# Kernel tuning notes

Measured on AMD Instinct MI355X. Metric: run time of the kernel, lower is better.

## Reference

```python
import jax, jax.numpy as jnp
import numpy as np

N_NODES = 100000


def _gcn_conv(h, src, dst, norm, W, b, n):
    # linear transform then symmetric-normalized scatter-add aggregation
    hw = h @ W                                   # [N, out]
    msg = hw[src] * norm[:, None]                # [E+N, out] gathered messages
    out = jax.ops.segment_sum(msg, dst, num_segments=n)
    return out + b


def _self_loops_and_norm(edge_index, n):
    loop = jnp.arange(n, dtype=edge_index.dtype)
    src = jnp.concatenate([edge_index[0], loop])
    dst = jnp.concatenate([edge_index[1], loop])
    deg = jax.ops.segment_sum(jnp.ones_like(src, dtype=jnp.float32), dst, num_segments=n)
    dinv = jnp.where(deg > 0, jax.lax.rsqrt(jnp.maximum(deg, 1.0)), 0.0)
    norm = dinv[src] * dinv[dst]                 # D^-1/2 (A+I) D^-1/2 coefficients
    return src, dst, norm


def setup_inputs() -> dict:
    key = jax.random.key(0)
    k1, k2, k3, k4 = jax.random.split(key, 4)
    F_IN, H, C = 128, 64, 40
    x = jax.random.normal(k1, (N_NODES, F_IN), dtype=jnp.float32)
    edge_index = jax.random.randint(k2, (2, 3200000), 0, N_NODES, dtype=jnp.int64)
    s1 = 1.0 / np.sqrt(F_IN)
    s2 = 1.0 / np.sqrt(H)
    W1 = jax.random.uniform(k3, (F_IN, H), jnp.float32, -s1, s1)
    b1 = jnp.zeros((H,), jnp.float32)
    W2 = jax.random.uniform(k4, (H, C), jnp.float32, -s2, s2)
    b2 = jnp.zeros((C,), jnp.float32)
    return {"x": x, "edge_index": edge_index, "W1": W1, "b1": b1, "W2": W2, "b2": b2}


def reference(x, edge_index, W1, b1, W2, b2):
    n = x.shape[0]
    src, dst, norm = _self_loops_and_norm(edge_index, n)
    h = _gcn_conv(x, src, dst, norm, W1, b1, n)
    h = jax.nn.relu(h)
    # dropout(p=0.5) is identity in eval mode
    out = _gcn_conv(h, src, dst, norm, W2, b2, n)
    return jax.nn.log_softmax(out, axis=1)
```

## Files before the change

kernel.cpp:

```cpp
#include <hip/hip_runtime.h>
#include <math.h>

#define F_IN 128
#define HID  64
#define NCLS 40
#define PART_CHUNK 4096
#define CAP 4608
#define CAPX 768
#define MAXNB 1024
#define ASTRIDE 132

typedef _Float16 half8 __attribute__((ext_vector_type(8)));
typedef _Float16 half2t __attribute__((ext_vector_type(2)));
typedef float floatx4 __attribute__((ext_vector_type(4)));

__device__ inline half8 ld_half8_u8(const _Float16* p) {
    union { uint2 u[2]; half8 h; } r;
    r.u[0] = *(const uint2*)p;
    r.u[1] = *(const uint2*)(p + 4);
    return r.h;
}

__global__ __launch_bounds__(256) void fused_part_gemm1(const int* __restrict__ src,
                                                        const int* __restrict__ dst,
                                                        int* __restrict__ bCur,
                                                        int* __restrict__ pkBuf,
                                                        int E, int NB, int nPart,
                                                        const float* __restrict__ x,
                                                        const float* __restrict__ W1,
                                                        _Float16* __restrict__ h1, int n) {
    __shared__ __align__(16) char smem[2 * 64 * ASTRIDE * 2];
    int tid = threadIdx.x;
    if ((int)blockIdx.x < nPart) {
        int xcd = (int)blockIdx.x & 7;
        int* hcnt  = (int*)smem;
        int* hbase = (int*)smem + MAXNB;
        for (int i = tid; i < NB; i += 256) hcnt[i] = 0;
        __syncthreads();
        int e0 = blockIdx.x * PART_CHUNK;
        int s_[16], d_[16];
#pragma unroll
        for (int i = 0; i < 16; ++i) {
            int e = e0 + i * 256 + tid;
            if (e < E) {
                s_[i] = src[e]; d_[i] = dst[e];
                atomicAdd(&hcnt[d_[i] >> 7], 1);
            }
        }
        __syncthreads();
        for (int b = tid; b < NB; b += 256) {
            int c = hcnt[b];
            hbase[b] = c ? ((b * 8 + xcd) * CAPX + atomicAdd(&bCur[b * 8 + xcd], c)) : 0;
            hcnt[b] = 0;
        }
        __syncthreads();
#pragma unroll
        for (int i = 0; i < 16; ++i) {
            int e = e0 + i * 256 + tid;
            if (e < E) {
                int b = d_[i] >> 7;
                int loc = atomicAdd(&hcnt[b], 1);
                pkBuf[hbase[b] + loc] = (s_[i] << 7) | (d_[i] & 127);
            }
        }
    } else {
        _Float16* Ah = (_Float16*)smem;
        _Float16* Wt = Ah + 64 * ASTRIDE;
        int node0 = ((int)blockIdx.x - nPart) * 64;
#pragma unroll
        for (int i = 0; i < 8; ++i) {
            int f = (i * 256 + tid) * 4;
            int m = f >> 7, k = f & 127;
            float4 v = (node0 + m < n) ? ((const float4*)(x + (size_t)(node0 + m) * F_IN))[k >> 2]
                                       : make_float4(0.f, 0.f, 0.f, 0.f);
            _Float16* p = &Ah[m * ASTRIDE + k];
            p[0] = (_Float16)v.x; p[1] = (_Float16)v.y; p[2] = (_Float16)v.z; p[3] = (_Float16)v.w;
        }
#pragma unroll
        for (int i = 0; i < 32; ++i) {
            int f = i * 256 + tid;
            int k = f >> 6, nn = f & 63;
            Wt[nn * ASTRIDE + k] = (_Float16)W1[f];
        }
        __syncthreads();
        int wave = tid >> 6, lane = tid & 63;
        int m0 = wave * 16;
        int col = lane & 15, quad = lane >> 4;
        floatx4 acc[4] = {{0,0,0,0},{0,0,0,0},{0,0,0,0},{0,0,0,0}};
#pragma unroll
        for (int kk = 0; kk < 4; ++kk) {
            int kbase = kk * 32 + quad * 8;
            half8 a = ld_half8_u8(&Ah[(m0 + col) * ASTRIDE + kbase]);
#pragma unroll
            for (int t = 0; t < 4; ++t) {
                half8 b = ld_half8_u8(&Wt[(t * 16 + col) * ASTRIDE + kbase]);
                acc[t] = __builtin_amdgcn_mfma_f32_16x16x32_f16(a, b, acc[t], 0, 0, 0);
            }
        }
#pragma unroll
        for (int t = 0; t < 4; ++t)
#pragma unroll
            for (int r = 0; r < 4; ++r) {
                int node = node0 + m0 + quad * 4 + r;
                if (node < n) h1[(size_t)node * HID + t * 16 + col] = (_Float16)acc[t][r];
            }
    }
}

__global__ __launch_bounds__(256) void scan_buckets(const int* __restrict__ bCur,
                                                    int* __restrict__ bBase, int NB, int E) {
    __shared__ int part[256];
    int tid = threadIdx.x;
    int v[4]; int sum = 0;
#pragma unroll
    for (int k = 0; k < 4; ++k) {
        int i = tid * 4 + k;
        int s = 0;
        if (i < NB) {
#pragma unroll
            for (int x = 0; x < 8; ++x) s += bCur[i * 8 + x];
        }
        v[k] = s;
        sum += s;
    }
    part[tid] = sum; __syncthreads();
    for (int off = 1; off < 256; off <<= 1) {
        int t = (tid >= off) ? part[tid - off] : 0;
        __syncthreads();
        part[tid] += t;
        __syncthreads();
    }
    int base = part[tid] - sum;
#pragma unroll
    for (int k = 0; k < 4; ++k) {
        int i = tid * 4 + k;
        if (i < NB) bBase[i] = base;
        base += v[k];
    }
    if (tid == 255) bBase[NB] = E;
}

__global__ __launch_bounds__(256) void bucket_finalize(const int* __restrict__ bCur,
                                                       const int* __restrict__ bBase,
                                                       const int* __restrict__ pkBuf,
                                                       int* __restrict__ ptr,
                                                       float* __restrict__ dinv,
                                                       int* __restrict__ sIdx,
                                                       _Float16* __restrict__ h1,
                                                       int n, int E) {
    __shared__ int cnt128[128];
    __shared__ int sc[128];
    __shared__ int cur[128];
    __shared__ float sdinv[128];
    __shared__ int segoff[9];
    __shared__ int ebuf[CAP];
    __shared__ int stage[CAP];
    int b = blockIdx.x;
    int node0 = b << 7;
    int tid = threadIdx.x;
    if (tid < 128) cnt128[tid] = 0;
    if (tid == 0) {
        int o = 0;
#pragma unroll
        for (int x = 0; x < 8; ++x) { segoff[x] = o; o += bCur[b * 8 + x]; }
        segoff[8] = o;
    }
    __syncthreads();
    int cnt = segoff[8];
    int dbase = bBase[b];
    for (int x = 0; x < 8; ++x) {
        int off = segoff[x], len = segoff[x + 1] - off;
        const int* s = pkBuf + (size_t)(b * 8 + x) * CAPX;
        for (int j = tid; j < len; j += 256) {
            int p = s[j];
            ebuf[off + j] = p;
            atomicAdd(&cnt128[p & 127], 1);
        }
    }
    __syncthreads();
    int v = (tid < 128) ? cnt128[tid] : 0;
    if (tid < 128) sc[tid] = v;
    __syncthreads();
    for (int off = 1; off < 128; off <<= 1) {
        int t = (tid < 128 && tid >= off) ? sc[tid - off] : 0;
        __syncthreads();
        if (tid < 128) sc[tid] += t;
        __syncthreads();
    }
    if (tid < 128) {
        cur[tid] = sc[tid] - v;
        float dv = rsqrtf((float)v + 1.0f);
        sdinv[tid] = dv;
        int node = node0 + tid;
        if (node < n) {
            ptr[node] = dbase + sc[tid] - v;
            dinv[node] = dv;
        }
    }
    if (tid == 0 && b == gridDim.x - 1) ptr[n] = E;
    __syncthreads();
    for (int j = tid; j < cnt; j += 256) {
        int p = ebuf[j];
        int pos = atomicAdd(&cur[p & 127], 1);
        stage[pos] = p >> 7;
    }
    __syncthreads();
    for (int j = tid; j < cnt; j += 256)
        sIdx[dbase + j] = stage[j];
#pragma unroll
    for (int pass = 0; pass < 4; ++pass) {
        int idx = pass * 256 + tid;
        int nd = node0 + (idx >> 3);
        if (nd < n) {
            float dv = sdinv[idx >> 3];
            half8* p = (half8*)(h1 + (size_t)nd * HID) + (idx & 7);
            half8 hv = *p;
#pragma unroll
            for (int j = 0; j < 8; ++j) hv[j] = (_Float16)((float)hv[j] * dv);
            *p = hv;
        }
    }
}

template<bool RELU>
__global__ __launch_bounds__(256) void gather4(const int* __restrict__ ptr,
                                               const int* __restrict__ sIdx,
                                               const float* __restrict__ dinv,
                                               const _Float16* __restrict__ hin,
                                               const float* __restrict__ bias,
                                               _Float16* __restrict__ hout, int n) {
    int tid = threadIdx.x, wave = tid >> 6, lane = tid & 63;
    int ng   = lane >> 4;
    int slot = (lane >> 3) & 1;
    int fq   = lane & 7;
    int node = blockIdx.x * 16 + wave * 4 + ng;
    bool valid = node < n;
    int nodeC = valid ? node : 0;
    int beg = ptr[nodeC];
    int end = valid ? ptr[nodeC + 1] : beg;
    float di = dinv[nodeC];
    float a0[8] = {0,0,0,0,0,0,0,0}, a1[8] = {0,0,0,0,0,0,0,0};

    if (slot == 0 && valid) {
        half8 v = *(const half8*)(hin + nodeC * HID + fq * 8);
#pragma unroll
        for (int j = 0; j < 8; ++j) a0[j] = (float)v[j];
    }
    const _Float16 ONE = (_Float16)1.0f, ZEROH = (_Float16)0.0f;
    for (int j0 = beg; j0 < end; j0 += 8) {
        int ja = j0 + slot, jb = j0 + 2 + slot, jc = j0 + 4 + slot, jd = j0 + 6 + slot;
        bool va = ja < end, vb = jb < end, vc = jc < end, vd = jd < end;
        int sa = sIdx[va ? ja : beg];
        int sb = sIdx[vb ? jb : beg];
        int sc_ = sIdx[vc ? jc : beg];
        int sd = sIdx[vd ? jd : beg];
        half8 ra = *(const half8*)(hin + sa * HID + fq * 8);
        half8 rb = *(const half8*)(hin + sb * HID + fq * 8);
        half8 rc = *(const half8*)(hin + sc_ * HID + fq * 8);
        half8 rd = *(const half8*)(hin + sd * HID + fq * 8);
#if __has_builtin(__builtin_amdgcn_fdot2)
        half2t wab = { va ? ONE : ZEROH, vb ? ONE : ZEROH };
        half2t wcd = { vc ? ONE : ZEROH, vd ? ONE : ZEROH };
#pragma unroll
        for (int j = 0; j < 8; ++j) {
            half2t pab = { ra[j], rb[j] };
            half2t pcd = { rc[j], rd[j] };
            a0[j] = __builtin_amdgcn_fdot2(pab, wab, a0[j], false);
            a1[j] = __builtin_amdgcn_fdot2(pcd, wcd, a1[j], false);
        }
#else
        float wa = va ? 1.f : 0.f, wb = vb ? 1.f : 0.f, wc = vc ? 1.f : 0.f, wd = vd ? 1.f : 0.f;
#pragma unroll
        for (int j = 0; j < 8; ++j) {
            a0[j] = fmaf((float)ra[j], wa, a0[j]);
            a0[j] = fmaf((float)rb[j], wb, a0[j]);
            a1[j] = fmaf((float)rc[j], wc, a1[j]);
            a1[j] = fmaf((float)rd[j], wd, a1[j]);
        }
#endif
    }
#pragma unroll
    for (int j = 0; j < 8; ++j) {
        a0[j] += a1[j];
        a0[j] += __shfl_xor(a0[j], 8, 64);
    }
    if (slot == 0 && valid) {
        union { half8 h; uint4 u; } o;
#pragma unroll
        for (int j = 0; j < 8; ++j) {
            float v = di * a0[j];
            if (RELU) v = fmaxf(v + bias[fq * 8 + j], 0.f) * di;
            o.h[j] = (_Float16)v;
        }
        *(uint4*)(hout + nodeC * HID + fq * 8) = o.u;
    }
}

#define GSTRIDE 72
__global__ __launch_bounds__(256) void gemm2_mfma_logsm(const _Float16* __restrict__ g,
                                                        const float* __restrict__ W2,
                                                        const float* __restrict__ b2,
                                                        float* __restrict__ out, int n) {
    __shared__ _Float16 gt[64 * GSTRIDE];
    __shared__ _Float16 wt[48 * GSTRIDE];
    int tid = threadIdx.x;
    int node0 = blockIdx.x * 64;
#pragma unroll
    for (int i = 0; i < 2; ++i) {
        int f = (i * 256 + tid) * 8;
        int m = f >> 6, k = f & 63;
        union { uint4 u; half8 h; } v;
        if (node0 + m < n) v.u = *(const uint4*)(g + (size_t)(node0 + m) * HID + k);
        else v.u = make_uint4(0, 0, 0, 0);
        *(uint4*)&gt[m * GSTRIDE + k] = v.u;
    }
#pragma unroll
    for (int i = 0; i < 12; ++i) {
        int f = i * 256 + tid;
        int c = f >> 6, k = f & 63;
        wt[c * GSTRIDE + k] = (c < NCLS) ? (_Float16)W2[k * NCLS + c] : (_Float16)0.f;
    }
    __syncthreads();

    int wave = tid >> 6, lane = tid & 63;
    int m0 = wave * 16;
    int col = lane & 15, quad = lane >> 4;
    floatx4 acc[3] = {{0,0,0,0},{0,0,0,0},{0,0,0,0}};
#pragma unroll
    for (int kk = 0; kk < 2; ++kk) {
        int kbase = kk * 32 + quad * 8;
        half8 a = *(const half8*)&gt[(m0 + col) * GSTRIDE + kbase];
#pragma unroll
        for (int t = 0; t < 3; ++t) {
            half8 b = *(const half8*)&wt[(t * 16 + col) * GSTRIDE + kbase];
            acc[t] = __builtin_amdgcn_mfma_f32_16x16x32_f16(a, b, acc[t], 0, 0, 0);
        }
    }
    float bb[3];
#pragma unroll
    for (int t = 0; t < 3; ++t) {
        int c = t * 16 + col;
        bb[t] = (c < NCLS) ? b2[c] : 0.f;
    }
#pragma unroll
    for (int r = 0; r < 4; ++r) {
        int node = node0 + m0 + quad * 4 + r;
        float v0 = acc[0][r] + bb[0];
        float v1 = acc[1][r] + bb[1];
        float v2 = (col < 8) ? acc[2][r] + bb[2] : -INFINITY;
        float m = fmaxf(fmaxf(v0, v1), v2);
#pragma unroll
        for (int off = 1; off < 16; off <<= 1) m = fmaxf(m, __shfl_xor(m, off, 64));
        float s = expf(v0 - m) + expf(v1 - m) + ((col < 8) ? expf(v2 - m) : 0.f);
#pragma unroll
        for (int off = 1; off < 16; off <<= 1) s += __shfl_xor(s, off, 64);
        float ls = logf(s);
        if (node < n) {
            float* op = out + (size_t)node * NCLS;
            op[col]      = v0 - m - ls;
            op[16 + col] = v1 - m - ls;
            if (col < 8) op[32 + col] = v2 - m - ls;
        }
    }
}

extern "C" void kernel_launch(void* const* d_in, const int* in_sizes, int n_in,
                              void* d_out, int out_size, void* d_ws, size_t ws_size,
                              hipStream_t stream) {
    const float* x  = (const float*)d_in[0];
    const int*   ei = (const int*)d_in[1];
    const float* W1 = (const float*)d_in[2];
    const float* b1 = (const float*)d_in[3];
    const float* W2 = (const float*)d_in[4];
    const float* b2 = (const float*)d_in[5];
    float* out = (float*)d_out;

    int n = in_sizes[0] / F_IN;
    int E = in_sizes[1] / 2;
    const int* src = ei;
    const int* dst = ei + E;
    int NB = (n + 127) >> 7;
    int nPart = (E + PART_CHUNK - 1) / PART_CHUNK;
    int nGemm1 = (n + 63) / 64;

    char* ws = (char*)d_ws;
    const size_t MB = 1024 * 1024;
    int*      bCur  = (int*)  (ws);
    int*      bBase = (int*)  (ws + 64 * 1024);
    int*      ptr   = (int*)  (ws + 128 * 1024);
    float*    dinv  = (float*)(ws + 1 * MB);
    int*      sIdx  = (int*)     (ws + 2 * MB);
    _Float16* bufA  = (_Float16*)(ws + 15 * MB);
    int*      pkBuf = (int*)     (ws + 28 * MB);
    _Float16* bufB  = (_Float16*)(ws + 28 * MB);

    hipMemsetAsync(bCur, 0, (size_t)NB * 8 * sizeof(int), stream);
    fused_part_gemm1<<<nPart + nGemm1, 256, 0, stream>>>(src, dst, bCur, pkBuf, E, NB, nPart,
                                                         x, W1, bufA, n);
    scan_buckets<<<1, 256, 0, stream>>>(bCur, bBase, NB, E);
    bucket_finalize<<<NB, 256, 0, stream>>>(bCur, bBase, pkBuf, ptr, dinv, sIdx, bufA, n, E);

    gather4<true ><<<(n + 15) / 16, 256, 0, stream>>>(ptr, sIdx, dinv, bufA, b1, bufB, n);
    gather4<false><<<(n + 15) / 16, 256, 0, stream>>>(ptr, sIdx, dinv, bufB, b1, bufA, n);
    gemm2_mfma_logsm<<<(n + 63) / 64, 256, 0, stream>>>(bufA, W2, b2, out, n);
}
```

Measured before the change: 299.6 us.

## Split hidden features into four 16-wide planes for cache-local gathers

Changes the hidden-feature buffer layout from node-major [N,64] to four feature planes [4][N][16]. GEMM1, the dinv scaling, and GEMM2 are updated to match. Each gather block now handles one plane, so the random-access working set per pass (about 3.2 MB) is meant to fit in L2/LLC. The cost is reading the edge index list four times per layer, partly offset by nontemporal loads of the index. The gather loop is also simplified, with edges split across four slots, a tail step, and a shuffle reduction.

```diff
diff --git a/kernel.cpp b/kernel.cpp
--- a/kernel.cpp
+++ b/kernel.cpp
@@ -13,6 +13,8 @@
 typedef _Float16 half8 __attribute__((ext_vector_type(8)));
 typedef _Float16 half2t __attribute__((ext_vector_type(2)));
 typedef float floatx4 __attribute__((ext_vector_type(4)));
+typedef unsigned int uint4v __attribute__((ext_vector_type(4)));
+
 
 __device__ inline half8 ld_half8_u8(const _Float16* p) {
     union { uint2 u[2]; half8 h; } r;
@@ -102,7 +104,7 @@
 #pragma unroll
             for (int r = 0; r < 4; ++r) {
                 int node = node0 + m0 + quad * 4 + r;
-                if (node < n) h1[(size_t)node * HID + t * 16 + col] = (_Float16)acc[t][r];
+                if (node < n) h1[((size_t)t * n + node) * 16 + col] = (_Float16)acc[t][r];
             }
     }
 }
@@ -208,91 +210,95 @@
     for (int j = tid; j < cnt; j += 256)
         sIdx[dbase + j] = stage[j];
 #pragma unroll
-    for (int pass = 0; pass < 4; ++pass) {
-        int idx = pass * 256 + tid;
-        int nd = node0 + (idx >> 3);
+    for (int it = 0; it < 2; ++it) {
+        int idx = it * 256 + tid;
+        int p = idx >> 7, ndl = idx & 127;
+        int nd = node0 + ndl;
         if (nd < n) {
-            float dv = sdinv[idx >> 3];
-            half8* p = (half8*)(h1 + (size_t)nd * HID) + (idx & 7);
-            half8 hv = *p;
-#pragma unroll
-            for (int j = 0; j < 8; ++j) hv[j] = (_Float16)((float)hv[j] * dv);
-            *p = hv;
+            float dv = sdinv[ndl];
+            _Float16* base = h1 + ((size_t)p * n + nd) * 16;
+            half8 a = *(half8*)base;
+            half8 c = *(half8*)(base + 8);
+#pragma unroll
+            for (int j = 0; j < 8; ++j) {
+                a[j] = (_Float16)((float)a[j] * dv);
+                c[j] = (_Float16)((float)c[j] * dv);
+            }
+            *(half8*)base = a;
+            *(half8*)(base + 8) = c;
         }
     }
 }
 
 template<bool RELU>
-__global__ __launch_bounds__(256) void gather4(const int* __restrict__ ptr,
-                                               const int* __restrict__ sIdx,
-                                               const float* __restrict__ dinv,
-                                               const _Float16* __restrict__ hin,
-                                               const float* __restrict__ bias,
-                                               _Float16* __restrict__ hout, int n) {
+__global__ __launch_bounds__(256) void gather_blk(const int* __restrict__ ptr,
+                                                  const int* __restrict__ sIdx,
+                                                  const float* __restrict__ dinv,
+                                                  const _Float16* __restrict__ hin,
+                                                  const float* __restrict__ bias,
+                                                  _Float16* __restrict__ hout,
+                                                  int n, int nblk) {
+    int bid = (int)blockIdx.x;
+    int p = bid / nblk;
+    int b = bid - p * nblk;
     int tid = threadIdx.x, wave = tid >> 6, lane = tid & 63;
-    int ng   = lane >> 4;
-    int slot = (lane >> 3) & 1;
-    int fq   = lane & 7;
-    int node = blockIdx.x * 16 + wave * 4 + ng;
+    int nd   = lane >> 3;
+    int slot = (lane >> 1) & 3;
+    int fl   = lane & 1;
+    int node = b * 32 + wave * 8 + nd;
     bool valid = node < n;
     int nodeC = valid ? node : 0;
     int beg = ptr[nodeC];
     int end = valid ? ptr[nodeC + 1] : beg;
     float di = dinv[nodeC];
-    float a0[8] = {0,0,0,0,0,0,0,0}, a1[8] = {0,0,0,0,0,0,0,0};
+    const _Float16* tbl = hin + (size_t)p * n * 16 + fl * 8;
+    float acc[8] = {0, 0, 0, 0, 0, 0, 0, 0};
 
     if (slot == 0 && valid) {
-        half8 v = *(const half8*)(hin + nodeC * HID + fq * 8);
-#pragma unroll
-        for (int j = 0; j < 8; ++j) a0[j] = (float)v[j];
-    }
-    const _Float16 ONE = (_Float16)1.0f, ZEROH = (_Float16)0.0f;
-    for (int j0 = beg; j0 < end; j0 += 8) {
-        int ja = j0 + slot, jb = j0 + 2 + slot, jc = j0 + 4 + slot, jd = j0 + 6 + slot;
-        bool va = ja < end, vb = jb < end, vc = jc < end, vd = jd < end;
-        int sa = sIdx[va ? ja : beg];
-        int sb = sIdx[vb ? jb : beg];
-        int sc_ = sIdx[vc ? jc : beg];
-        int sd = sIdx[vd ? jd : beg];
-        half8 ra = *(const half8*)(hin + sa * HID + fq * 8);
-        half8 rb = *(const half8*)(hin + sb * HID + fq * 8);
-        half8 rc = *(const half8*)(hin + sc_ * HID + fq * 8);
-        half8 rd = *(const half8*)(hin + sd * HID + fq * 8);
+        half8 v = *(const half8*)(tbl + (size_t)nodeC * 16);
+#pragma unroll
+        for (int j = 0; j < 8; ++j) acc[j] = (float)v[j];
+    }
+    int j = beg + slot;
 #if __has_builtin(__builtin_amdgcn_fdot2)
-        half2t wab = { va ? ONE : ZEROH, vb ? ONE : ZEROH };
-        half2t wcd = { vc ? ONE : ZEROH, vd ? ONE : ZEROH };
-#pragma unroll
-        for (int j = 0; j < 8; ++j) {
-            half2t pab = { ra[j], rb[j] };
-            half2t pcd = { rc[j], rd[j] };
-            a0[j] = __builtin_amdgcn_fdot2(pab, wab, a0[j], false);
-            a1[j] = __builtin_amdgcn_fdot2(pcd, wcd, a1[j], false);
+    const half2t ONE2 = { (_Float16)1.0f, (_Float16)1.0f };
+#endif
+    for (; j + 4 < end; j += 8) {
+        int s1 = __builtin_nontemporal_load(&sIdx[j]);
+        int s2 = __builtin_nontemporal_load(&sIdx[j + 4]);
+        half8 r1 = *(const half8*)(tbl + (size_t)s1 * 16);
+        half8 r2 = *(const half8*)(tbl + (size_t)s2 * 16);
+#if __has_builtin(__builtin_amdgcn_fdot2)
+#pragma unroll
+        for (int jj = 0; jj < 8; ++jj) {
+            half2t pr = { r1[jj], r2[jj] };
+            acc[jj] = __builtin_amdgcn_fdot2(pr, ONE2, acc[jj], false);
         }
 #else
-        float wa = va ? 1.f : 0.f, wb = vb ? 1.f : 0.f, wc = vc ? 1.f : 0.f, wd = vd ? 1.f : 0.f;
-#pragma unroll
-        for (int j = 0; j < 8; ++j) {
-            a0[j] = fmaf((float)ra[j], wa, a0[j]);
-            a0[j] = fmaf((float)rb[j], wb, a0[j]);
-            a1[j] = fmaf((float)rc[j], wc, a1[j]);
-            a1[j] = fmaf((float)rd[j], wd, a1[j]);
-        }
+#pragma unroll
+        for (int jj = 0; jj < 8; ++jj) acc[jj] += (float)r1[jj] + (float)r2[jj];
 #endif
     }
-#pragma unroll
-    for (int j = 0; j < 8; ++j) {
-        a0[j] += a1[j];
-        a0[j] += __shfl_xor(a0[j], 8, 64);
+    if (j < end) {
+        int s1 = __builtin_nontemporal_load(&sIdx[j]);
+        half8 r1 = *(const half8*)(tbl + (size_t)s1 * 16);
+#pragma unroll
+        for (int jj = 0; jj < 8; ++jj) acc[jj] += (float)r1[jj];
+    }
+#pragma unroll
+    for (int jj = 0; jj < 8; ++jj) {
+        acc[jj] += __shfl_xor(acc[jj], 2, 64);
+        acc[jj] += __shfl_xor(acc[jj], 4, 64);
     }
     if (slot == 0 && valid) {
-        union { half8 h; uint4 u; } o;
-#pragma unroll
-        for (int j = 0; j < 8; ++j) {
-            float v = di * a0[j];
-            if (RELU) v = fmaxf(v + bias[fq * 8 + j], 0.f) * di;
-            o.h[j] = (_Float16)v;
-        }
-        *(uint4*)(hout + nodeC * HID + fq * 8) = o.u;
+        union { half8 h; uint4v u; } o;
+#pragma unroll
+        for (int jj = 0; jj < 8; ++jj) {
+            float v = di * acc[jj];
+            if (RELU) v = fmaxf(v + bias[p * 16 + fl * 8 + jj], 0.f) * di;
+            o.h[jj] = (_Float16)v;
+        }
+        __builtin_nontemporal_store(o.u, (uint4v*)(hout + ((size_t)p * n + nodeC) * 16 + fl * 8));
     }
 }
 
@@ -309,8 +315,9 @@
     for (int i = 0; i < 2; ++i) {
         int f = (i * 256 + tid) * 8;
         int m = f >> 6, k = f & 63;
+        int p = k >> 4, off = k & 15;
         union { uint4 u; half8 h; } v;
-        if (node0 + m < n) v.u = *(const uint4*)(g + (size_t)(node0 + m) * HID + k);
+        if (node0 + m < n) v.u = *(const uint4*)(g + ((size_t)p * n + node0 + m) * 16 + off);
         else v.u = make_uint4(0, 0, 0, 0);
         *(uint4*)&gt[m * GSTRIDE + k] = v.u;
     }
@@ -382,6 +389,7 @@
     int NB = (n + 127) >> 7;
     int nPart = (E + PART_CHUNK - 1) / PART_CHUNK;
     int nGemm1 = (n + 63) / 64;
+    int nblkG = (n + 31) / 32;
 
     char* ws = (char*)d_ws;
     const size_t MB = 1024 * 1024;
@@ -400,7 +408,7 @@
     scan_buckets<<<1, 256, 0, stream>>>(bCur, bBase, NB, E);
     bucket_finalize<<<NB, 256, 0, stream>>>(bCur, bBase, pkBuf, ptr, dinv, sIdx, bufA, n, E);
 
-    gather4<true ><<<(n + 15) / 16, 256, 0, stream>>>(ptr, sIdx, dinv, bufA, b1, bufB, n);
-    gather4<false><<<(n + 15) / 16, 256, 0, stream>>>(ptr, sIdx, dinv, bufB, b1, bufA, n);
+    gather_blk<true ><<<4 * nblkG, 256, 0, stream>>>(ptr, sIdx, dinv, bufA, b1, bufB, n, nblkG);
+    gather_blk<false><<<4 * nblkG, 256, 0, stream>>>(ptr, sIdx, dinv, bufB, b1, bufA, n, nblkG);
     gemm2_mfma_logsm<<<(n + 63) / 64, 256, 0, stream>>>(bufA, W2, b2, out, n);
 }
```

Result: slower. 427.4 us (+42.6%).
